# Kernel tuning notes

Hardware: AMD Instinct MI355X
Metric: run time of the kernel (lower is better)

Reference implementation:

```python
import jax, jax.numpy as jnp
import numpy as np

N = 100000        # num_nodes
E_HALF = 800000   # directed edges; full symmetric edge list has 2*E_HALF
D = 64            # feature dim (hard-coded Linear(64,64) in source)
STEP = 1.0        # step_size


def setup_inputs() -> dict:
    key = jax.random.key(0)
    k1, k2, k3, k4, k5, k6 = jax.random.split(key, 6)
    src = jax.random.randint(k1, (E_HALF,), 0, N)
    dst = jax.random.randint(k2, (E_HALF,), 0, N)
    # symmetric edge list: edge e in [0,E_HALF) has its reverse at e+E_HALF
    edge_index = jnp.stack([jnp.concatenate([src, dst]),
                            jnp.concatenate([dst, src])])  # (2, 2*E_HALF)
    left_idx = jnp.arange(2 * E_HALF)
    right_idx = jnp.concatenate([jnp.arange(E_HALF, 2 * E_HALF),
                                 jnp.arange(0, E_HALF)])
    x = jax.random.normal(k3, (N, D), dtype=jnp.float32)
    W_sheaf = jax.random.normal(k4, (1, 2 * D), dtype=jnp.float32) * 0.08  # sheaf_learner (128->1, no bias)
    W_lin = jax.random.normal(k5, (D, D), dtype=jnp.float32) * 0.125       # linear 64->64
    b_lin = jax.random.normal(k6, (D,), dtype=jnp.float32) * 0.01
    return {"x": x, "W_sheaf": W_sheaf, "W_lin": W_lin, "b_lin": b_lin,
            "edge_index": edge_index, "left_idx": left_idx, "right_idx": right_idx}


def reference(x, W_sheaf, W_lin, b_lin, edge_index, left_idx, right_idx):
    row, col = edge_index[0], edge_index[1]
    # predict_restriction_maps: gather endpoints, concat, linear, tanh -> (E,1)
    x_row = x[row]
    x_col = x[col]
    maps = jnp.tanh(jnp.concatenate([x_row, x_col], axis=1) @ W_sheaf.T)  # (E,1)
    # build_laplacian
    left_maps = maps[left_idx]
    right_maps = maps[right_idx]
    non_diag_maps = -left_maps * right_maps                                # (E,1)
    diag_maps = jax.ops.segment_sum(maps ** 2, row, num_segments=N)       # (N,1)
    d_sqrt_inv = jax.lax.rsqrt(diag_maps + 1.0)                            # (N,1)
    norm_maps = d_sqrt_inv[row] * non_diag_maps * d_sqrt_inv[col]          # (E,1)
    diag = d_sqrt_inv * diag_maps * d_sqrt_inv                             # (N,1)
    # y = linear(x); sparse Laplacian @ y = diag part + scatter-add of edge part
    y = x @ W_lin.T + b_lin                                                # (N,D)
    Ly = diag * y + jax.ops.segment_sum(norm_maps * y[col], row, num_segments=N)
    return x - STEP * Ly
```

## Files before the change

kernel.cpp:

```cpp
#include <hip/hip_runtime.h>
#include <hip/hip_fp16.h>


#define NBLK_BIN 256
#define CHUNK_CAP 4096
#define STAGE_CAP 8192

__global__ __launch_bounds__(256) void k_pre_hist(
    const float* __restrict__ x,
    const float* __restrict__ Wsheaf,
    const float* __restrict__ Wlin,
    const float* __restrict__ blin,
    float2* __restrict__ s12,
    __half* __restrict__ yz,
    const int* __restrict__ row, const int* __restrict__ col,
    unsigned* __restrict__ table,
    int N, int Eh, int NB, int NPRE)
{
    __shared__ float4 xt[64 * 16];
    int tid = threadIdx.x;

    if (blockIdx.x >= NPRE) {
        unsigned* h = (unsigned*)xt;
        int hb = blockIdx.x - NPRE;
        for (int i = tid; i < NB; i += 256) h[i] = 0;
        __syncthreads();
        int chunk = (Eh + NBLK_BIN - 1) / NBLK_BIN;
        int lo = hb * chunk, hi = min(lo + chunk, Eh);
        for (int i = lo + tid; i < hi; i += 256) {
            atomicAdd(&h[(unsigned)row[i] >> 8], 1u);
            atomicAdd(&h[(unsigned)col[i] >> 8], 1u);
        }
        __syncthreads();
        for (int i = tid; i < NB; i += 256) table[(size_t)hb * NB + i] = h[i];
        return;
    }

    int lane = tid & 63;
    int wave = tid >> 6;
    int n0   = blockIdx.x * 64;

    float wreg[64];
    {
        const float4* Wv = (const float4*)(Wlin + lane * 64);
        #pragma unroll
        for (int q = 0; q < 16; ++q) {
            float4 w4 = Wv[q];
            wreg[4 * q + 0] = w4.x; wreg[4 * q + 1] = w4.y;
            wreg[4 * q + 2] = w4.z; wreg[4 * q + 3] = w4.w;
        }
    }
    float bl  = blin[lane];
    float ws1 = Wsheaf[lane];
    float ws2 = Wsheaf[64 + lane];

    int nvalid = min(64, N - n0);
    const float4* xg = (const float4*)(x + (size_t)n0 * 64);
    for (int i = tid; i < nvalid * 16; i += 256) xt[i] = xg[i];
    __syncthreads();

    int ni_end = min(wave * 16 + 16, nvalid);
    for (int ni = wave * 16; ni < ni_end; ++ni) {
        float xv = ((const float*)xt)[ni * 64 + lane];
        float a = xv * ws1, b = xv * ws2;
        #pragma unroll
        for (int m = 32; m; m >>= 1) {
            a += __shfl_xor(a, m);
            b += __shfl_xor(b, m);
        }
        if (lane == 0) s12[n0 + ni] = make_float2(a, b);

        float acc = bl;
        #pragma unroll
        for (int q = 0; q < 16; ++q) {
            float4 xq = xt[ni * 16 + q];
            acc += xq.x * wreg[4 * q + 0] + xq.y * wreg[4 * q + 1]
                 + xq.z * wreg[4 * q + 2] + xq.w * wreg[4 * q + 3];
        }
        yz[(size_t)(n0 + ni) * 64 + lane] = __float2half(acc);
    }
}

__global__ __launch_bounds__(256) void k_colscan(
    unsigned* __restrict__ table, unsigned* __restrict__ colsum, int NB)
{
    __shared__ unsigned sm[256];
    int j = blockIdx.x, t = threadIdx.x;
    unsigned v = table[(size_t)t * NB + j];
    sm[t] = v;
    __syncthreads();
    for (int off = 1; off < 256; off <<= 1) {
        unsigned u = (t >= off) ? sm[t - off] : 0;
        __syncthreads();
        if (t >= off) sm[t] += u;
        __syncthreads();
    }
    table[(size_t)t * NB + j] = sm[t] - v;
    if (t == 255) colsum[j] = sm[255];
}

__global__ __launch_bounds__(512, 1) void k_binplace(
    const float2* __restrict__ s12,
    const int* __restrict__ row, const int* __restrict__ col,
    const unsigned* __restrict__ table, const unsigned* __restrict__ colsum,
    uint2* __restrict__ binned, int Eh, int NB)
{
    __shared__ unsigned csum[512];
    __shared__ unsigned destbase[512];
    __shared__ unsigned h[512];
    __shared__ unsigned locex[512];
    __shared__ unsigned cur[512];
    __shared__ uint2    stg[STAGE_CAP];
    __shared__ unsigned gaddr[STAGE_CAP];
    __shared__ __half2  pm[CHUNK_CAP];

    int t = threadIdx.x;

    unsigned v = (t < NB) ? colsum[t] : 0;
    csum[t] = v;
    __syncthreads();
    for (int off = 1; off < 512; off <<= 1) {
        unsigned u = (t >= off) ? csum[t - off] : 0;
        __syncthreads();
        csum[t] += u;
        __syncthreads();
    }
    if (t < NB) destbase[t] = (csum[t] - v) + table[(size_t)blockIdx.x * NB + t];
    h[t] = 0;
    cur[t] = 0;
    __syncthreads();

    int chunk = (Eh + NBLK_BIN - 1) / NBLK_BIN;
    int lo = blockIdx.x * chunk, hi = min(lo + chunk, Eh);

    if (chunk <= CHUNK_CAP) {
        for (int i = lo + t; i < hi; i += 512) {
            int r = row[i], c = col[i];
            float2 sr = s12[r], sc2 = s12[c];
            float mf = tanhf(sr.x + sc2.y);
            float mr = tanhf(sc2.x + sr.y);
            pm[i - lo] = __halves2half2(__float2half_rn(mf), __float2half_rn(mr));
            atomicAdd(&h[(unsigned)r >> 8], 1u);
            atomicAdd(&h[(unsigned)c >> 8], 1u);
        }
        __syncthreads();
        unsigned hv = h[t];
        csum[t] = hv;
        __syncthreads();
        for (int off = 1; off < 512; off <<= 1) {
            unsigned u = (t >= off) ? csum[t - off] : 0;
            __syncthreads();
            csum[t] += u;
            __syncthreads();
        }
        locex[t] = csum[t] - hv;
        __syncthreads();
        for (int i = lo + t; i < hi; i += 512) {
            int r = row[i], c = col[i];
            __half2 m = pm[i - lo];
            float mf = __low2float(m), mr = __high2float(m);
            float pr = mf * mr;

            unsigned bk_r = (unsigned)r >> 8;
            unsigned pos1 = atomicAdd(&cur[bk_r], 1u);
            unsigned s1i  = locex[bk_r] + pos1;
            __half2 h1 = __halves2half2(__float2half_rn(mf * mf), __float2half_rn(pr));
            stg[s1i]   = make_uint2(((unsigned)(r & 255) << 17) | (unsigned)c,
                                    *reinterpret_cast<unsigned*>(&h1));
            gaddr[s1i] = destbase[bk_r] + pos1;

            unsigned bk_c = (unsigned)c >> 8;
            unsigned pos2 = atomicAdd(&cur[bk_c], 1u);
            unsigned s2i  = locex[bk_c] + pos2;
            __half2 h2 = __halves2half2(__float2half_rn(mr * mr), __float2half_rn(pr));
            stg[s2i]   = make_uint2(((unsigned)(c & 255) << 17) | (unsigned)r,
                                    *reinterpret_cast<unsigned*>(&h2));
            gaddr[s2i] = destbase[bk_c] + pos2;
        }
        __syncthreads();
        int total = (hi > lo) ? 2 * (hi - lo) : 0;
        for (int i = t; i < total; i += 512) binned[gaddr[i]] = stg[i];
    } else {
        for (int i = lo + t; i < hi; i += 512) {
            int r = row[i], c = col[i];
            float2 sr = s12[r], sc2 = s12[c];
            float mf = tanhf(sr.x + sc2.y);
            float mr = tanhf(sc2.x + sr.y);
            float pr = mf * mr;
            __half2 h1 = __halves2half2(__float2half_rn(mf * mf), __float2half_rn(pr));
            unsigned bk_r = (unsigned)r >> 8;
            unsigned d1 = destbase[bk_r] + atomicAdd(&cur[bk_r], 1u);
            binned[d1] = make_uint2(((unsigned)(r & 255) << 17) | (unsigned)c,
                                    *reinterpret_cast<unsigned*>(&h1));
            __half2 h2 = __halves2half2(__float2half_rn(mr * mr), __float2half_rn(pr));
            unsigned bk_c = (unsigned)c >> 8;
            unsigned d2 = destbase[bk_c] + atomicAdd(&cur[bk_c], 1u);
            binned[d2] = make_uint2(((unsigned)(c & 255) << 17) | (unsigned)r,
                                    *reinterpret_cast<unsigned*>(&h2));
        }
    }
}

__global__ __launch_bounds__(256) void k_bucket(
    const uint2* __restrict__ binned,
    const unsigned* __restrict__ colsum,
    int* __restrict__ base, float* __restrict__ dinv,
    int2* __restrict__ sc,
    __half* __restrict__ yz,
    int N, int NB)
{
    __shared__ unsigned cnt[256];
    __shared__ float dsum[256];
    __shared__ unsigned pref[256];
    __shared__ unsigned cur[256];
    __shared__ float sdinv[256];
    __shared__ unsigned red[256];

    int b = blockIdx.x, t = threadIdx.x;
    int row0 = b << 8;

    unsigned part = 0;
    for (int j = t; j < b; j += 256) part += colsum[j];
    red[t] = part;
    cnt[t] = 0;
    dsum[t] = 0.0f;
    __syncthreads();
    for (int m = 128; m; m >>= 1) {
        if (t < m) red[t] += red[t + m];
        __syncthreads();
    }
    int lo = (int)red[0];
    int hi = lo + (int)colsum[b];

    for (int i = lo + t; i < hi; i += 256) {
        uint2 v = binned[i];
        unsigned rl = v.x >> 17;
        atomicAdd(&cnt[rl], 1u);
        __half2 h = *reinterpret_cast<__half2*>(&v.y);
        atomicAdd(&dsum[rl], __low2float(h));
    }
    __syncthreads();

    unsigned myc = cnt[t];
    pref[t] = myc;
    __syncthreads();
    for (int off = 1; off < 256; off <<= 1) {
        unsigned u = (t >= off) ? pref[t - off] : 0;
        __syncthreads();
        if (t >= off) pref[t] += u;
        __syncthreads();
    }
    unsigned excl = pref[t] - myc;
    float dv = rsqrtf(dsum[t] + 1.0f);
    sdinv[t] = dv;
    int rown = row0 + t;
    if (rown < N) {
        base[rown] = lo + (int)excl;
        dinv[rown] = dv;
    }
    if (b == (int)gridDim.x - 1 && t == 0) base[N] = hi;
    cur[t] = excl;
    __syncthreads();

    for (int i = lo + t; i < hi; i += 256) {
        uint2 v = binned[i];
        unsigned rl = v.x >> 17;
        unsigned other = v.x & 0x1FFFFu;
        unsigned slot = (unsigned)lo + atomicAdd(&cur[rl], 1u);
        __half2 h = *reinterpret_cast<__half2*>(&v.y);
        sc[slot] = make_int2((int)other, __float_as_int(__high2float(h)));
    }

    __half2* yz2 = (__half2*)yz;
    for (int i = t; i < 256 * 32; i += 256) {
        int rl = i >> 5;
        int rn = row0 + rl;
        if (rn < N) {
            size_t idx = (size_t)rn * 32 + (i & 31);
            __half2 v = yz2[idx];
            float s = sdinv[rl];
            yz2[idx] = __floats2half2_rn(s * __low2float(v), s * __high2float(v));
        }
    }
}

__global__ __launch_bounds__(256) void k_node_gather(
    const float* __restrict__ x,
    const __half* __restrict__ zh,
    const float* __restrict__ dinv,
    const int* __restrict__ base,
    const int2* __restrict__ sc,
    float* __restrict__ out,
    int N)
{
    __shared__ int2 stage[4][64];
    int lane = threadIdx.x & 63;
    int wave = threadIdx.x >> 6;
    int n = blockIdx.x * 4 + wave;
    if (n >= N) return;

    int j0 = base[n], end = base[n + 1];
    float acc = 0.0f;
    for (int blk = j0; blk < end; blk += 64) {
        int m = min(64, end - blk);
        if (lane < m) stage[wave][lane] = sc[blk + lane];
        #pragma unroll 4
        for (int j = 0; j < m; ++j) {
            int2 r = stage[wave][j];
            acc += __int_as_float(r.y) * __half2float(zh[(size_t)r.x * 64 + lane]);
        }
    }
    float dv = dinv[n];
    int idx = n * 64 + lane;
    float zv = __half2float(zh[idx]);
    out[idx] = x[idx] - (1.0f / dv - dv) * zv + dv * acc;
}

extern "C" void kernel_launch(void* const* d_in, const int* in_sizes, int n_in,
                              void* d_out, int out_size, void* d_ws, size_t ws_size,
                              hipStream_t stream) {
    const float* x      = (const float*)d_in[0];
    const float* Wsheaf = (const float*)d_in[1];
    const float* Wlin   = (const float*)d_in[2];
    const float* blin   = (const float*)d_in[3];
    const int*   ei     = (const int*)d_in[4];
    float* out = (float*)d_out;

    int N  = in_sizes[0] / 64;
    int E  = in_sizes[4] / 2;
    int Eh = E >> 1;
    int NB = (N + 255) >> 8;
    int NPRE = (N + 63) / 64;
    const int* row = ei;
    const int* col = ei + E;

    char* ws = (char*)d_ws;
    float2*   s12    = (float2*)ws;             ws += (size_t)N * 8;
    uint2*    binned = (uint2*)ws;              ws += (size_t)E * 8;
    int2*     sc     = (int2*)ws;               ws += (size_t)E * 8;
    unsigned* table  = (unsigned*)ws;           ws += (size_t)NBLK_BIN * NB * 4;
    unsigned* colsum = (unsigned*)ws;           ws += (size_t)NB * 4;
    int*      base   = (int*)ws;                ws += (size_t)(N + 1) * 4;
    float*    dinv   = (float*)ws;              ws += (size_t)N * 4;
    __half*   yz     = (__half*)ws;             ws += (size_t)N * 64 * 2;

    k_pre_hist <<<NPRE + NBLK_BIN, 256, 0, stream>>>(x, Wsheaf, Wlin, blin, s12, yz,
                                                     row, col, table, N, Eh, NB, NPRE);
    k_colscan  <<<NB, 256, 0, stream>>>(table, colsum, NB);
    k_binplace <<<NBLK_BIN, 512, 0, stream>>>(s12, row, col, table, colsum, binned, Eh, NB);
    k_bucket   <<<NB, 256, 0, stream>>>(binned, colsum, base, dinv, sc, yz, N, NB);
    k_node_gather<<<(N + 3) / 4, 256, 0, stream>>>(x, yz, dinv, base, sc, out, N);
}
```

Before: 246.7 us.

## Double binning blocks, drop gaddr staging, widen bucket blocks, half2 gather

Doubles the number of binning blocks and halves the per-block chunk and stage sizes. It replaces the stored per-entry global address with a binary search over the local bucket offsets at flush time, which saves shared memory so more blocks can be resident. It also moves k_bucket to 512-thread blocks and changes the node gather so each wave processes two edges at once with half2 loads, combined by a cross-half shuffle. The costs are the extra binary-search work per flushed entry, more histogram table rows to scan, and idle threads in parts of k_bucket.

```diff
diff --git a/kernel.cpp b/kernel.cpp
--- a/kernel.cpp
+++ b/kernel.cpp
@@ -2,9 +2,9 @@
 #include <hip/hip_fp16.h>
 
 
-#define NBLK_BIN 256
-#define CHUNK_CAP 4096
-#define STAGE_CAP 8192
+#define NBLK_BIN 512
+#define CHUNK_CAP 2048
+#define STAGE_CAP 4096
 
 __global__ __launch_bounds__(256) void k_pre_hist(
     const float* __restrict__ x,
@@ -81,25 +81,25 @@
     }
 }
 
-__global__ __launch_bounds__(256) void k_colscan(
+__global__ __launch_bounds__(512) void k_colscan(
     unsigned* __restrict__ table, unsigned* __restrict__ colsum, int NB)
 {
-    __shared__ unsigned sm[256];
+    __shared__ unsigned sm[512];
     int j = blockIdx.x, t = threadIdx.x;
     unsigned v = table[(size_t)t * NB + j];
     sm[t] = v;
     __syncthreads();
-    for (int off = 1; off < 256; off <<= 1) {
+    for (int off = 1; off < 512; off <<= 1) {
         unsigned u = (t >= off) ? sm[t - off] : 0;
         __syncthreads();
         if (t >= off) sm[t] += u;
         __syncthreads();
     }
     table[(size_t)t * NB + j] = sm[t] - v;
-    if (t == 255) colsum[j] = sm[255];
-}
-
-__global__ __launch_bounds__(512, 1) void k_binplace(
+    if (t == 511) colsum[j] = sm[511];
+}
+
+__global__ __launch_bounds__(512) void k_binplace(
     const float2* __restrict__ s12,
     const int* __restrict__ row, const int* __restrict__ col,
     const unsigned* __restrict__ table, const unsigned* __restrict__ colsum,
@@ -108,10 +108,9 @@
     __shared__ unsigned csum[512];
     __shared__ unsigned destbase[512];
     __shared__ unsigned h[512];
-    __shared__ unsigned locex[512];
+    __shared__ unsigned locex[513];
     __shared__ unsigned cur[512];
     __shared__ uint2    stg[STAGE_CAP];
-    __shared__ unsigned gaddr[STAGE_CAP];
     __shared__ __half2  pm[CHUNK_CAP];
 
     int t = threadIdx.x;
@@ -154,6 +153,7 @@
             __syncthreads();
         }
         locex[t] = csum[t] - hv;
+        if (t == 511) locex[512] = csum[511];
         __syncthreads();
         for (int i = lo + t; i < hi; i += 512) {
             int r = row[i], c = col[i];
@@ -163,23 +163,26 @@
 
             unsigned bk_r = (unsigned)r >> 8;
             unsigned pos1 = atomicAdd(&cur[bk_r], 1u);
-            unsigned s1i  = locex[bk_r] + pos1;
             __half2 h1 = __halves2half2(__float2half_rn(mf * mf), __float2half_rn(pr));
-            stg[s1i]   = make_uint2(((unsigned)(r & 255) << 17) | (unsigned)c,
-                                    *reinterpret_cast<unsigned*>(&h1));
-            gaddr[s1i] = destbase[bk_r] + pos1;
+            stg[locex[bk_r] + pos1] = make_uint2(((unsigned)(r & 255) << 17) | (unsigned)c,
+                                                 *reinterpret_cast<unsigned*>(&h1));
 
             unsigned bk_c = (unsigned)c >> 8;
             unsigned pos2 = atomicAdd(&cur[bk_c], 1u);
-            unsigned s2i  = locex[bk_c] + pos2;
             __half2 h2 = __halves2half2(__float2half_rn(mr * mr), __float2half_rn(pr));
-            stg[s2i]   = make_uint2(((unsigned)(c & 255) << 17) | (unsigned)r,
-                                    *reinterpret_cast<unsigned*>(&h2));
-            gaddr[s2i] = destbase[bk_c] + pos2;
+            stg[locex[bk_c] + pos2] = make_uint2(((unsigned)(c & 255) << 17) | (unsigned)r,
+                                                 *reinterpret_cast<unsigned*>(&h2));
         }
         __syncthreads();
         int total = (hi > lo) ? 2 * (hi - lo) : 0;
-        for (int i = t; i < total; i += 512) binned[gaddr[i]] = stg[i];
+        for (int i = t; i < total; i += 512) {
+            int loB = 0, hiB = NB;
+            while (hiB - loB > 1) {
+                int mid = (loB + hiB) >> 1;
+                if (locex[mid] <= (unsigned)i) loB = mid; else hiB = mid;
+            }
+            binned[destbase[loB] + ((unsigned)i - locex[loB])] = stg[i];
+        }
     } else {
         for (int i = lo + t; i < hi; i += 512) {
             int r = row[i], c = col[i];
@@ -201,7 +204,7 @@
     }
 }
 
-__global__ __launch_bounds__(256) void k_bucket(
+__global__ __launch_bounds__(512) void k_bucket(
     const uint2* __restrict__ binned,
     const unsigned* __restrict__ colsum,
     int* __restrict__ base, float* __restrict__ dinv,
@@ -214,25 +217,24 @@
     __shared__ unsigned pref[256];
     __shared__ unsigned cur[256];
     __shared__ float sdinv[256];
-    __shared__ unsigned red[256];
+    __shared__ unsigned red[512];
 
     int b = blockIdx.x, t = threadIdx.x;
     int row0 = b << 8;
 
     unsigned part = 0;
-    for (int j = t; j < b; j += 256) part += colsum[j];
+    for (int j = t; j < b; j += 512) part += colsum[j];
     red[t] = part;
-    cnt[t] = 0;
-    dsum[t] = 0.0f;
-    __syncthreads();
-    for (int m = 128; m; m >>= 1) {
+    if (t < 256) { cnt[t] = 0; dsum[t] = 0.0f; }
+    __syncthreads();
+    for (int m = 256; m; m >>= 1) {
         if (t < m) red[t] += red[t + m];
         __syncthreads();
     }
     int lo = (int)red[0];
     int hi = lo + (int)colsum[b];
 
-    for (int i = lo + t; i < hi; i += 256) {
+    for (int i = lo + t; i < hi; i += 512) {
         uint2 v = binned[i];
         unsigned rl = v.x >> 17;
         atomicAdd(&cnt[rl], 1u);
@@ -241,28 +243,31 @@
     }
     __syncthreads();
 
-    unsigned myc = cnt[t];
-    pref[t] = myc;
+    unsigned myc = (t < 256) ? cnt[t] : 0;
+    if (t < 256) pref[t] = myc;
     __syncthreads();
     for (int off = 1; off < 256; off <<= 1) {
-        unsigned u = (t >= off) ? pref[t - off] : 0;
-        __syncthreads();
-        if (t >= off) pref[t] += u;
-        __syncthreads();
-    }
-    unsigned excl = pref[t] - myc;
-    float dv = rsqrtf(dsum[t] + 1.0f);
-    sdinv[t] = dv;
-    int rown = row0 + t;
-    if (rown < N) {
-        base[rown] = lo + (int)excl;
-        dinv[rown] = dv;
+        unsigned u = 0;
+        if (t < 256 && t >= off) u = pref[t - off];
+        __syncthreads();
+        if (t < 256 && t >= off) pref[t] += u;
+        __syncthreads();
+    }
+    if (t < 256) {
+        unsigned excl = pref[t] - myc;
+        float dv = rsqrtf(dsum[t] + 1.0f);
+        sdinv[t] = dv;
+        int rown = row0 + t;
+        if (rown < N) {
+            base[rown] = lo + (int)excl;
+            dinv[rown] = dv;
+        }
+        cur[t] = excl;
     }
     if (b == (int)gridDim.x - 1 && t == 0) base[N] = hi;
-    cur[t] = excl;
-    __syncthreads();
-
-    for (int i = lo + t; i < hi; i += 256) {
+    __syncthreads();
+
+    for (int i = lo + t; i < hi; i += 512) {
         uint2 v = binned[i];
         unsigned rl = v.x >> 17;
         unsigned other = v.x & 0x1FFFFu;
@@ -272,7 +277,7 @@
     }
 
     __half2* yz2 = (__half2*)yz;
-    for (int i = t; i < 256 * 32; i += 256) {
+    for (int i = t; i < 256 * 32; i += 512) {
         int rl = i >> 5;
         int rn = row0 + rl;
         if (rn < N) {
@@ -299,21 +304,38 @@
     int n = blockIdx.x * 4 + wave;
     if (n >= N) return;
 
+    int g = lane >> 5;
+    int l = lane & 31;
+    const __half2* zh2 = (const __half2*)zh;
+
     int j0 = base[n], end = base[n + 1];
-    float acc = 0.0f;
+    float accx = 0.0f, accy = 0.0f;
     for (int blk = j0; blk < end; blk += 64) {
         int m = min(64, end - blk);
         if (lane < m) stage[wave][lane] = sc[blk + lane];
-        #pragma unroll 4
-        for (int j = 0; j < m; ++j) {
-            int2 r = stage[wave][j];
-            acc += __int_as_float(r.y) * __half2float(zh[(size_t)r.x * 64 + lane]);
-        }
-    }
-    float dv = dinv[n];
-    int idx = n * 64 + lane;
-    float zv = __half2float(zh[idx]);
-    out[idx] = x[idx] - (1.0f / dv - dv) * zv + dv * acc;
+        for (int j = 0; j < m; j += 2) {
+            int jj = j + g;
+            int2 r = stage[wave][(jj < m) ? jj : j];
+            float coeff = (jj < m) ? __int_as_float(r.y) : 0.0f;
+            float2 vf = __half22float2(zh2[(size_t)r.x * 32 + l]);
+            accx += coeff * vf.x;
+            accy += coeff * vf.y;
+        }
+    }
+    accx += __shfl_xor(accx, 32);
+    accy += __shfl_xor(accy, 32);
+
+    if (g == 0) {
+        float dv = dinv[n];
+        float s = 1.0f / dv - dv;
+        size_t idx = (size_t)n * 64 + 2 * l;
+        float2 xv = *(const float2*)(x + idx);
+        float2 zf = __half22float2(zh2[(size_t)n * 32 + l]);
+        float2 o;
+        o.x = xv.x - s * zf.x + dv * accx;
+        o.y = xv.y - s * zf.y + dv * accy;
+        *(float2*)(out + idx) = o;
+    }
 }
 
 extern "C" void kernel_launch(void* const* d_in, const int* in_sizes, int n_in,
@@ -346,8 +368,8 @@
 
     k_pre_hist <<<NPRE + NBLK_BIN, 256, 0, stream>>>(x, Wsheaf, Wlin, blin, s12, yz,
                                                      row, col, table, N, Eh, NB, NPRE);
-    k_colscan  <<<NB, 256, 0, stream>>>(table, colsum, NB);
+    k_colscan  <<<NB, 512, 0, stream>>>(table, colsum, NB);
     k_binplace <<<NBLK_BIN, 512, 0, stream>>>(s12, row, col, table, colsum, binned, Eh, NB);
-    k_bucket   <<<NB, 256, 0, stream>>>(binned, colsum, base, dinv, sc, yz, N, NB);
+    k_bucket   <<<NB, 512, 0, stream>>>(binned, colsum, base, dinv, sc, yz, N, NB);
     k_node_gather<<<(N + 3) / 4, 256, 0, stream>>>(x, yz, dinv, base, sc, out, N);
 }
```

New measurement: 259.7 us. 1.05x slower.
